# Performance work log

Measured on AMD Instinct MI355X. Metric: run time of the kernel, lower is better.

Reference implementation:

```python
import jax, jax.numpy as jnp
import numpy as np

BLOCK = 64      # sparse block size (power of 2, >= 16)
NB = 128        # number of blocks -> max_seqlen = 8192
LOCAL = 8       # causal local window, in blocks
GLOBAL = 1      # leading global blocks every query attends to
K = LOCAL + GLOBAL
SM_SCALE = 1.0 / np.sqrt(64.0)  # default sm_scale = 1/sqrt(head_dim)


def _build_layout():
    # Fixed-width equivalent of the CSR block layout: for query block i,
    # live key blocks are the GLOBAL leading blocks plus the LOCAL-wide
    # causal window ending at i. Entries outside [0, i] are masked invalid;
    # global entries that fall inside the local window are invalidated to
    # avoid double counting.
    rows = np.arange(NB)[:, None]
    loc = rows - np.arange(LOCAL - 1, -1, -1)[None, :]      # [NB, LOCAL], ascending, ends at i
    glb = np.tile(np.arange(GLOBAL)[None, :], (NB, 1))      # [NB, GLOBAL]
    loc_valid = loc >= 0
    glb_valid = glb < (rows - LOCAL + 1)                    # strictly below local window
    col = np.concatenate([glb, np.maximum(loc, 0)], axis=1)  # [NB, K]
    valid = np.concatenate([glb_valid, loc_valid], axis=1)   # [NB, K]
    return col.astype(np.int32), valid


def setup_inputs() -> dict:
    key = jax.random.key(0)
    kq, kk, kv = jax.random.split(key, 3)
    B, S, H, D = 2, NB * BLOCK, 16, 64
    q = jax.random.normal(kq, (B, S, H, D), jnp.float32)
    k = jax.random.normal(kk, (B, S, H, D), jnp.float32)
    v = jax.random.normal(kv, (B, S, H, D), jnp.float32)
    col, valid = _build_layout()
    return {"q": q, "k": k, "v": v,
            "col_idx": jnp.asarray(col), "col_valid": jnp.asarray(valid)}


def reference(q, k, v, col_idx, col_valid):
    # Block-sparse causal attention. Only key/value blocks listed in
    # col_idx (where col_valid) are touched; token-level causal mask is
    # applied inside the gathered blocks (diagonal blocks get intra-block
    # causal masking, matching the kernel's behavior).
    B, S, H, D = q.shape
    bs = BLOCK
    nb = S // bs
    qb = q.reshape(B, nb, bs, H, D)                       # [B, nb, bs, H, D]
    kb = k.reshape(B, nb, bs, H, D)[:, col_idx]           # [B, nb, K, bs, H, D]
    vb = v.reshape(B, nb, bs, H, D)[:, col_idx]
    scores = jnp.einsum('bimhd,bijnhd->bhimjn', qb, kb) * SM_SCALE  # [B,H,nb,bs,K,bs]
    qpos = jnp.arange(nb)[:, None] * bs + jnp.arange(bs)[None, :]          # [nb, bs]
    kpos = col_idx[:, :, None] * bs + jnp.arange(bs)[None, None, :]        # [nb, K, bs]
    mask = (kpos[:, None, :, :] <= qpos[:, :, None, None]) & col_valid[:, None, :, None]
    neg = jnp.finfo(scores.dtype).min
    scores = jnp.where(mask[None, None], scores, neg)
    shp = scores.shape
    p = jax.nn.softmax(scores.reshape(shp[0], shp[1], shp[2], shp[3], -1), axis=-1).reshape(shp)
    out = jnp.einsum('bhimjn,bijnhd->bimhd', p, vb)       # [B, nb, bs, H, D]
    return out.reshape(B, S, H, D)
```

## Files before the change

kernel.cpp:

```cpp
#include <hip/hip_runtime.h>
#include <hip/hip_bf16.h>

#define BLOCKSZ 64
#define NBQ     128
#define NLOCAL  8
#define NH      16
#define NBATCH  2
#define DIM     64
#define SEQ     (NBQ * BLOCKSZ)
#define KPAD    72
#define QK_SCALE 0.1803368801111204f

typedef __attribute__((ext_vector_type(8))) short bf16x8;
typedef __attribute__((ext_vector_type(4))) short short4v;
typedef __attribute__((ext_vector_type(4))) float f32x4;

__device__ inline short f2b(float x) {
    unsigned int u = __float_as_uint(x);
    return (short)((u + 0x8000u) >> 16);
}

__global__ __launch_bounds__(256) void sparse_attn_kernel(
    const float* __restrict__ Q, const float* __restrict__ Kg,
    const float* __restrict__ Vg, float* __restrict__ Out)
{
    __shared__ __align__(16) short sK [64 * KPAD];
    __shared__ __align__(16) short sVt[64 * KPAD];
    __shared__ __align__(16) short sP [4 * 16 * KPAD];

    const int qb  = blockIdx.x >> 5;
    const int bh  = blockIdx.x & 31;
    const int b   = bh >> 4;
    const int h   = bh & 15;
    const int tid  = threadIdx.x;
    const int wave = tid >> 6;
    const int lane = tid & 63;
    const int quad = lane >> 4;
    const int l15  = lane & 15;

    bf16x8 qf[2];
    {
        const int qrow = qb * 64 + wave * 16 + l15;
        const float* qp = Q + (((size_t)(b * SEQ + qrow)) * NH + h) * DIM;
#pragma unroll
        for (int ks = 0; ks < 2; ++ks) {
            const float* p = qp + ks * 32 + quad * 8;
            const f32x4 x0 = *(const f32x4*)(p);
            const f32x4 x1 = *(const f32x4*)(p + 4);
            bf16x8 f;
#pragma unroll
            for (int c = 0; c < 4; ++c) {
                f[c]     = f2b(x0[c] * QK_SCALE);
                f[c + 4] = f2b(x1[c] * QK_SCALE);
            }
            qf[ks] = f;
        }
    }

    float l_part[4];
    f32x4 o_acc[4];
#pragma unroll
    for (int r = 0; r < 4; ++r) l_part[r] = 0.f;
#pragma unroll
    for (int ft = 0; ft < 4; ++ft) o_acc[ft] = (f32x4){0.f, 0.f, 0.f, 0.f};

    const int token_s = tid >> 2;
    const int f4_s    = (tid & 3) << 2;

    for (int j = 0; j < 9; ++j) {
        int kb; bool valid;
        if (j == 0) { kb = 0; valid = (qb >= NLOCAL); }
        else        { kb = qb - 8 + j; valid = (kb >= 0); }
        if (!valid) continue;
        const bool diag = (kb == qb);

        {
            const size_t basek = (((size_t)(b * SEQ + kb * 64 + token_s)) * NH + h) * DIM;
#pragma unroll
            for (int r = 0; r < 4; ++r) {
                const int f0 = f4_s + 16 * r;
                const f32x4 kx = *(const f32x4*)(Kg + basek + f0);
                const f32x4 vx = *(const f32x4*)(Vg + basek + f0);
                short4v kp;
                kp[0] = f2b(kx[0]); kp[1] = f2b(kx[1]); kp[2] = f2b(kx[2]); kp[3] = f2b(kx[3]);
                *(short4v*)&sK[token_s * KPAD + f0] = kp;
                sVt[(f0 + 0) * KPAD + token_s] = f2b(vx[0]);
                sVt[(f0 + 1) * KPAD + token_s] = f2b(vx[1]);
                sVt[(f0 + 2) * KPAD + token_s] = f2b(vx[2]);
                sVt[(f0 + 3) * KPAD + token_s] = f2b(vx[3]);
            }
        }
        __syncthreads();

        f32x4 s[4];
#pragma unroll
        for (int nt = 0; nt < 4; ++nt) {
            const bf16x8 k0 = *(const bf16x8*)&sK[(nt * 16 + l15) * KPAD + quad * 8];
            const bf16x8 k1 = *(const bf16x8*)&sK[(nt * 16 + l15) * KPAD + 32 + quad * 8];
            f32x4 acc = (f32x4){0.f, 0.f, 0.f, 0.f};
            acc = __builtin_amdgcn_mfma_f32_16x16x32_bf16(qf[0], k0, acc, 0, 0, 0);
            acc = __builtin_amdgcn_mfma_f32_16x16x32_bf16(qf[1], k1, acc, 0, 0, 0);
            s[nt] = acc;
        }

        bf16x8 vf[8];
#pragma unroll
        for (int ft = 0; ft < 4; ++ft) {
            vf[2 * ft]     = *(const bf16x8*)&sVt[(ft * 16 + l15) * KPAD + quad * 8];
            vf[2 * ft + 1] = *(const bf16x8*)&sVt[(ft * 16 + l15) * KPAD + 32 + quad * 8];
        }

        if (diag) {
#pragma unroll
            for (int nt = 0; nt < 4; ++nt) {
                const int ki = nt * 16 + l15;
#pragma unroll
                for (int r = 0; r < 4; ++r) {
                    const int qi = wave * 16 + quad * 4 + r;
                    if (ki > qi) s[nt][r] = -1e30f;
                }
            }
        }

#pragma unroll
        for (int r = 0; r < 4; ++r) {
            float ps = 0.f;
#pragma unroll
            for (int nt = 0; nt < 4; ++nt) {
                const float p = exp2f(s[nt][r]);
                s[nt][r] = p;
                ps += p;
            }
            l_part[r] += ps;
        }

        short* pbase = &sP[wave * 16 * KPAD];
#pragma unroll
        for (int nt = 0; nt < 4; ++nt)
#pragma unroll
            for (int r = 0; r < 4; ++r)
                pbase[(quad * 4 + r) * KPAD + nt * 16 + l15] = f2b(s[nt][r]);
        __syncthreads();
        const bf16x8 pf0 = *(const bf16x8*)&pbase[l15 * KPAD + quad * 8];
        const bf16x8 pf1 = *(const bf16x8*)&pbase[l15 * KPAD + 32 + quad * 8];

#pragma unroll
        for (int ft = 0; ft < 4; ++ft) {
            o_acc[ft] = __builtin_amdgcn_mfma_f32_16x16x32_bf16(pf0, vf[2 * ft],     o_acc[ft], 0, 0, 0);
            o_acc[ft] = __builtin_amdgcn_mfma_f32_16x16x32_bf16(pf1, vf[2 * ft + 1], o_acc[ft], 0, 0, 0);
        }
    }

#pragma unroll
    for (int r = 0; r < 4; ++r) {
        float l = l_part[r];
        l += __shfl_xor(l, 1);
        l += __shfl_xor(l, 2);
        l += __shfl_xor(l, 4);
        l += __shfl_xor(l, 8);
        const float inv = 1.0f / l;
        const int qrow = qb * 64 + wave * 16 + quad * 4 + r;
        float* op = Out + (((size_t)(b * SEQ + qrow)) * NH + h) * DIM;
#pragma unroll
        for (int ft = 0; ft < 4; ++ft)
            op[ft * 16 + l15] = o_acc[ft][r] * inv;
    }
}

extern "C" void kernel_launch(void* const* d_in, const int* in_sizes, int n_in,
                              void* d_out, int out_size, void* d_ws, size_t ws_size,
                              hipStream_t stream) {
    const float* q = (const float*)d_in[0];
    const float* k = (const float*)d_in[1];
    const float* v = (const float*)d_in[2];
    float* out = (float*)d_out;
    dim3 grid(NBQ * NBATCH * NH);
    sparse_attn_kernel<<<grid, dim3(256), 0, stream>>>(q, k, v, out);
}
```

Baseline: 276.3 us.

## Stage K/V as 4x4 register tiles with XOR-swizzled LDS and packed V transpose

Each thread now loads a 4-token by 4-feature tile of K and V, packs bf16 pairs with v_perm, and writes 8-byte words. This replaces the 2-byte scalar transpose stores into sVt. The padded LDS rows become unpadded 64-wide rows with an XOR swizzle on 4-element groups, and the MFMA fragment reads are adjusted to match. The aim is to cut LDS store instruction count and bank conflicts in the staging phase. In exchange, the global loads are less contiguous per thread and the fragment addressing gets more complex.

```diff
diff --git a/kernel.cpp b/kernel.cpp
--- a/kernel.cpp
+++ b/kernel.cpp
@@ -1,32 +1,34 @@
 #include <hip/hip_runtime.h>
 #include <hip/hip_bf16.h>
 
-#define BLOCKSZ 64
 #define NBQ     128
 #define NLOCAL  8
 #define NH      16
 #define NBATCH  2
 #define DIM     64
-#define SEQ     (NBQ * BLOCKSZ)
-#define KPAD    72
+#define SEQ     (NBQ * 64)
+#define PPAD    72
 #define QK_SCALE 0.1803368801111204f
 
 typedef __attribute__((ext_vector_type(8))) short bf16x8;
-typedef __attribute__((ext_vector_type(4))) short short4v;
 typedef __attribute__((ext_vector_type(4))) float f32x4;
+typedef __attribute__((ext_vector_type(2))) unsigned int u32x2;
 
 __device__ inline short f2b(float x) {
     unsigned int u = __float_as_uint(x);
     return (short)((u + 0x8000u) >> 16);
+}
+__device__ inline unsigned int pack2(unsigned int lo_rnd, unsigned int hi_rnd) {
+    return __builtin_amdgcn_perm(hi_rnd, lo_rnd, 0x07060302u);
 }
 
 __global__ __launch_bounds__(256) void sparse_attn_kernel(
     const float* __restrict__ Q, const float* __restrict__ Kg,
     const float* __restrict__ Vg, float* __restrict__ Out)
 {
-    __shared__ __align__(16) short sK [64 * KPAD];
-    __shared__ __align__(16) short sVt[64 * KPAD];
-    __shared__ __align__(16) short sP [4 * 16 * KPAD];
+    __shared__ __align__(16) short sK [64 * 64];
+    __shared__ __align__(16) short sVt[64 * 64];
+    __shared__ __align__(16) short sP [4 * 16 * PPAD];
 
     const int qb  = blockIdx.x >> 5;
     const int bh  = blockIdx.x & 31;
@@ -38,6 +40,11 @@
     const int quad = lane >> 4;
     const int l15  = lane & 15;
 
+    const int sg   = tid >> 4;
+    const int t15c = tid & 15;
+    const int tok4 = sg << 2;
+    const int ft4  = t15c << 2;
+
     bf16x8 qf[2];
     {
         const int qrow = qb * 64 + wave * 16 + l15;
@@ -64,8 +71,7 @@
 #pragma unroll
     for (int ft = 0; ft < 4; ++ft) o_acc[ft] = (f32x4){0.f, 0.f, 0.f, 0.f};
 
-    const int token_s = tid >> 2;
-    const int f4_s    = (tid & 3) << 2;
+    const int gsw = l15 & 14;
 
     for (int j = 0; j < 9; ++j) {
         int kb; bool valid;
@@ -75,19 +81,35 @@
         const bool diag = (kb == qb);
 
         {
-            const size_t basek = (((size_t)(b * SEQ + kb * 64 + token_s)) * NH + h) * DIM;
-#pragma unroll
-            for (int r = 0; r < 4; ++r) {
-                const int f0 = f4_s + 16 * r;
-                const f32x4 kx = *(const f32x4*)(Kg + basek + f0);
-                const f32x4 vx = *(const f32x4*)(Vg + basek + f0);
-                short4v kp;
-                kp[0] = f2b(kx[0]); kp[1] = f2b(kx[1]); kp[2] = f2b(kx[2]); kp[3] = f2b(kx[3]);
-                *(short4v*)&sK[token_s * KPAD + f0] = kp;
-                sVt[(f0 + 0) * KPAD + token_s] = f2b(vx[0]);
-                sVt[(f0 + 1) * KPAD + token_s] = f2b(vx[1]);
-                sVt[(f0 + 2) * KPAD + token_s] = f2b(vx[2]);
-                sVt[(f0 + 3) * KPAD + token_s] = f2b(vx[3]);
+            const size_t basekv = (((size_t)(b * SEQ + kb * 64 + tok4)) * NH + h) * DIM + ft4;
+            unsigned int kr[4][4], vr[4][4];
+#pragma unroll
+            for (int i = 0; i < 4; ++i) {
+                const f32x4 kx = *(const f32x4*)(Kg + basekv + (size_t)i * (NH * DIM));
+                const f32x4 vx = *(const f32x4*)(Vg + basekv + (size_t)i * (NH * DIM));
+#pragma unroll
+                for (int c = 0; c < 4; ++c) {
+                    kr[i][c] = __float_as_uint(kx[c]) + 0x8000u;
+                    vr[i][c] = __float_as_uint(vx[c]) + 0x8000u;
+                }
+            }
+#pragma unroll
+            for (int i = 0; i < 4; ++i) {
+                const int row = tok4 + i;
+                const int cp  = t15c ^ (row & 14);
+                u32x2 w;
+                w.x = pack2(kr[i][0], kr[i][1]);
+                w.y = pack2(kr[i][2], kr[i][3]);
+                *(u32x2*)&sK[row * 64 + cp * 4] = w;
+            }
+#pragma unroll
+            for (int c = 0; c < 4; ++c) {
+                const int row = ft4 + c;
+                const int cp  = sg ^ (row & 14);
+                u32x2 w;
+                w.x = pack2(vr[0][c], vr[1][c]);
+                w.y = pack2(vr[2][c], vr[3][c]);
+                *(u32x2*)&sVt[row * 64 + cp * 4] = w;
             }
         }
         __syncthreads();
@@ -95,8 +117,9 @@
         f32x4 s[4];
 #pragma unroll
         for (int nt = 0; nt < 4; ++nt) {
-            const bf16x8 k0 = *(const bf16x8*)&sK[(nt * 16 + l15) * KPAD + quad * 8];
-            const bf16x8 k1 = *(const bf16x8*)&sK[(nt * 16 + l15) * KPAD + 32 + quad * 8];
+            const int row = (nt * 16 + l15) * 64;
+            const bf16x8 k0 = *(const bf16x8*)&sK[row + (((quad * 2)     ^ gsw) << 2)];
+            const bf16x8 k1 = *(const bf16x8*)&sK[row + (((8 + quad * 2) ^ gsw) << 2)];
             f32x4 acc = (f32x4){0.f, 0.f, 0.f, 0.f};
             acc = __builtin_amdgcn_mfma_f32_16x16x32_bf16(qf[0], k0, acc, 0, 0, 0);
             acc = __builtin_amdgcn_mfma_f32_16x16x32_bf16(qf[1], k1, acc, 0, 0, 0);
@@ -106,8 +129,9 @@
         bf16x8 vf[8];
 #pragma unroll
         for (int ft = 0; ft < 4; ++ft) {
-            vf[2 * ft]     = *(const bf16x8*)&sVt[(ft * 16 + l15) * KPAD + quad * 8];
-            vf[2 * ft + 1] = *(const bf16x8*)&sVt[(ft * 16 + l15) * KPAD + 32 + quad * 8];
+            const int row = (ft * 16 + l15) * 64;
+            vf[2 * ft]     = *(const bf16x8*)&sVt[row + (((quad * 2)     ^ gsw) << 2)];
+            vf[2 * ft + 1] = *(const bf16x8*)&sVt[row + (((8 + quad * 2) ^ gsw) << 2)];
         }
 
         if (diag) {
@@ -134,15 +158,15 @@
             l_part[r] += ps;
         }
 
-        short* pbase = &sP[wave * 16 * KPAD];
+        short* pbase = &sP[wave * 16 * PPAD];
 #pragma unroll
         for (int nt = 0; nt < 4; ++nt)
 #pragma unroll
             for (int r = 0; r < 4; ++r)
-                pbase[(quad * 4 + r) * KPAD + nt * 16 + l15] = f2b(s[nt][r]);
+                pbase[(quad * 4 + r) * PPAD + nt * 16 + l15] = f2b(s[nt][r]);
         __syncthreads();
-        const bf16x8 pf0 = *(const bf16x8*)&pbase[l15 * KPAD + quad * 8];
-        const bf16x8 pf1 = *(const bf16x8*)&pbase[l15 * KPAD + 32 + quad * 8];
+        const bf16x8 pf0 = *(const bf16x8*)&pbase[l15 * PPAD + quad * 8];
+        const bf16x8 pf1 = *(const bf16x8*)&pbase[l15 * PPAD + 32 + quad * 8];
 
 #pragma unroll
         for (int ft = 0; ft < 4; ++ft) {
```

After: 261.1 us. 5.5% less time.
